# Kernel tuning notes

Hardware: AMD Instinct MI355X
Metric: run time of the kernel (lower is better)

Reference implementation:

```python
import jax, jax.numpy as jnp
import numpy as np

D_MODEL = 1024
NHEAD = 16
WINDOW = 128


def setup_inputs() -> dict:
    key = jax.random.key(0)
    ks = jax.random.split(key, 7)
    B, L, D = 4, 4096, D_MODEL
    s = 0.02
    return {
        "q": jax.random.normal(ks[0], (B, L, D), jnp.float32),
        "k": jax.random.normal(ks[1], (B, L, D), jnp.float32),
        "v": jax.random.normal(ks[2], (B, L, D), jnp.float32),
        "in_proj_w": jax.random.normal(ks[3], (3 * D, D), jnp.float32) * s,
        "in_proj_b": jnp.zeros((3 * D,), jnp.float32),
        "out_w": jax.random.normal(ks[4], (D, D), jnp.float32) * s,
        "out_b": jnp.zeros((D,), jnp.float32),
    }


def reference(q, k, v, in_proj_w, in_proj_b, out_w, out_b):
    B, L, D = q.shape
    H, W = NHEAD, WINDOW
    hd = D // H
    nW = L // W
    Wq, Wk, Wv = in_proj_w[:D], in_proj_w[D:2 * D], in_proj_w[2 * D:]
    bq, bk, bv = in_proj_b[:D], in_proj_b[D:2 * D], in_proj_b[2 * D:]
    # shared per-window projections (same weights every window, as in nn.MultiheadAttention)
    qp = (q @ Wq.T + bq).reshape(B, nW, W, H, hd)
    kp = (k @ Wk.T + bk).reshape(B, nW, W, H, hd)
    vp = (v @ Wv.T + bv).reshape(B, nW, W, H, hd)
    scale = 1.0 / np.sqrt(hd).astype(np.float32)
    # block-diagonal attention: scores only within each window n
    scores = jnp.einsum("bnqhd,bnkhd->bnhqk", qp, kp) * scale  # [B,nW,H,W,W]
    attn = jax.nn.softmax(scores, axis=-1)
    out = jnp.einsum("bnhqk,bnkhd->bnqhd", attn, vp).reshape(B, L, D)
    return out @ out_w.T + out_b
```

## Files before the change

### kernel.cpp

```cpp
#include <hip/hip_runtime.h>

#define M_TOK 16384
#define DM    1024

typedef __bf16 bf16x8 __attribute__((ext_vector_type(8)));
typedef float  f32x4  __attribute__((ext_vector_type(4)));
typedef unsigned short us8 __attribute__((ext_vector_type(8)));
typedef unsigned short us4 __attribute__((ext_vector_type(4)));

__device__ __forceinline__ unsigned short f2bf(float f) {
    unsigned u = __float_as_uint(f);
    u += 0x7FFFu + ((u >> 16) & 1u);
    return (unsigned short)(u >> 16);
}

__device__ __forceinline__ void gl2lds16(const unsigned short* g, unsigned short* l) {
    __builtin_amdgcn_global_load_lds(
        (const __attribute__((address_space(1))) unsigned int*)g,
        (__attribute__((address_space(3))) unsigned int*)l, 16, 0, 0);
}

__global__ __launch_bounds__(256) void conv_f2b(
    const float* __restrict__ src, unsigned short* __restrict__ dst, int n8)
{
    int i = blockIdx.x * blockDim.x + threadIdx.x;
    int stride = gridDim.x * blockDim.x;
    for (; i < n8; i += stride) {
        const float4* s = (const float4*)(src + (size_t)i * 8);
        float4 a = s[0], b = s[1];
        us8 o;
        o[0] = f2bf(a.x); o[1] = f2bf(a.y); o[2] = f2bf(a.z); o[3] = f2bf(a.w);
        o[4] = f2bf(b.x); o[5] = f2bf(b.y); o[6] = f2bf(b.z); o[7] = f2bf(b.w);
        *(us8*)(dst + (size_t)i * 8) = o;
    }
}

#define GEMM_CORE(A_, B_)                                                      \
    __shared__ unsigned short As[4096];                                        \
    __shared__ unsigned short Bs[4096];                                        \
    const int tid = threadIdx.x, lane = tid & 63, wv = tid >> 6;               \
    const int wrow = (wv >> 1) * 64, wcol = (wv & 1) * 64;                     \
    const int lrow = lane & 15, qd = lane >> 4;                                \
    const int mbase = blockIdx.y * 128, nbase = blockIdx.x * 128;              \
    const int s0 = tid, s1 = tid + 256;                                        \
    const int r0 = s0 >> 2, c0 = (s0 & 3) ^ ((r0 >> 1) & 3);                   \
    const int r1 = s1 >> 2, c1 = (s1 & 3) ^ ((r1 >> 1) & 3);                   \
    const int g0 = r0 * DM + c0 * 8;                                           \
    const int g1 = r1 * DM + c1 * 8;                                           \
    int aslot[4], bslot[4];                                                    \
    _Pragma("unroll")                                                          \
    for (int i = 0; i < 4; ++i) {                                              \
        int ra = wrow + i * 16 + lrow;                                         \
        int rb = wcol + i * 16 + lrow;                                         \
        aslot[i] = ra * 32 + (qd ^ ((ra >> 1) & 3)) * 8;                       \
        bslot[i] = rb * 32 + (qd ^ ((rb >> 1) & 3)) * 8;                       \
    }                                                                          \
    const unsigned short* Ab = (A_) + (size_t)mbase * DM;                      \
    const unsigned short* Bb = (B_) + (size_t)nbase * DM;                      \
    f32x4 acc[4][4] = {};                                                      \
    for (int k0 = 0; k0 < DM; k0 += 32) {                                      \
        __syncthreads();                                                       \
        gl2lds16(Ab + k0 + g0, As + s0 * 8);                                   \
        gl2lds16(Ab + k0 + g1, As + s1 * 8);                                   \
        gl2lds16(Bb + k0 + g0, Bs + s0 * 8);                                   \
        gl2lds16(Bb + k0 + g1, Bs + s1 * 8);                                   \
        __syncthreads();                                                       \
        bf16x8 af[4], bfr[4];                                                  \
        _Pragma("unroll")                                                      \
        for (int i = 0; i < 4; ++i) af[i]  = *(const bf16x8*)(As + aslot[i]);  \
        _Pragma("unroll")                                                      \
        for (int i = 0; i < 4; ++i) bfr[i] = *(const bf16x8*)(Bs + bslot[i]);  \
        _Pragma("unroll")                                                      \
        for (int i = 0; i < 4; ++i)                                            \
            _Pragma("unroll")                                                  \
            for (int j = 0; j < 4; ++j)                                        \
                acc[i][j] = __builtin_amdgcn_mfma_f32_16x16x32_bf16(           \
                    af[i], bfr[j], acc[i][j], 0, 0, 0);                        \
    }

__global__ __launch_bounds__(256) void gemm_bt_qkv(
    const unsigned short* __restrict__ A, const unsigned short* __restrict__ W,
    const float* __restrict__ bias, unsigned short* __restrict__ C, int z)
{
    GEMM_CORE(A, W)
    if (z <= 1) {
        #pragma unroll
        for (int j = 0; j < 4; ++j) {
            int gc = nbase + wcol + j * 16 + lrow;
            int h = gc >> 6, dh = gc & 63;
            float bv = bias[gc];
            #pragma unroll
            for (int i = 0; i < 4; ++i) {
                int gr0 = mbase + wrow + i * 16 + qd * 4;
                int b = gr0 >> 12;
                #pragma unroll
                for (int r = 0; r < 4; ++r) {
                    int tok = (gr0 + r) & 4095;
                    C[(((size_t)b * 16 + h) * 4096 + tok) * 64 + dh] =
                        f2bf(acc[i][j][r] + bv);
                }
            }
        }
    } else {
        #pragma unroll
        for (int j = 0; j < 4; ++j) {
            int gc = nbase + wcol + j * 16 + lrow;
            int h = gc >> 6, dh = gc & 63;
            float bv = bias[gc];
            #pragma unroll
            for (int i = 0; i < 4; ++i) {
                int gr0 = mbase + wrow + i * 16 + qd * 4;
                int b = gr0 >> 12, tok = gr0 & 4095;
                us4 pk;
                #pragma unroll
                for (int r = 0; r < 4; ++r) pk[r] = f2bf(acc[i][j][r] + bv);
                *(us4*)(C + (((size_t)b * 16 + h) * 64 + dh) * 4096 + tok) = pk;
            }
        }
    }
}

__global__ __launch_bounds__(256) void gemm_bt_out(
    const unsigned short* __restrict__ A, const unsigned short* __restrict__ W,
    const float* __restrict__ bias, float* __restrict__ out)
{
    GEMM_CORE(A, W)
    #pragma unroll
    for (int j = 0; j < 4; ++j) {
        int gc = nbase + wcol + j * 16 + lrow;
        float bv = bias[gc];
        #pragma unroll
        for (int i = 0; i < 4; ++i) {
            int gr0 = mbase + wrow + i * 16 + qd * 4;
            #pragma unroll
            for (int r = 0; r < 4; ++r)
                out[(size_t)(gr0 + r) * DM + gc] = acc[i][j][r] + bv;
        }
    }
}

__global__ __launch_bounds__(256) void attn_v2(
    const unsigned short* __restrict__ qh, const unsigned short* __restrict__ kh,
    const unsigned short* __restrict__ vt, unsigned short* __restrict__ aout)
{
    const int gid = blockIdx.x;
    const int h  = gid & 15;
    const int wi = (gid >> 4) & 31;
    const int b  = gid >> 9;
    const int bh = b * 16 + h;

    const unsigned short* Qp = qh + ((size_t)bh * 4096 + wi * 128) * 64;
    const unsigned short* Kp = kh + ((size_t)bh * 4096 + wi * 128) * 64;
    const unsigned short* Vp = vt + (size_t)bh * 64 * 4096 + wi * 128;

    const int tid = threadIdx.x, lane = tid & 63, wv = tid >> 6;
    const int lrow = lane & 15, qd = lane >> 4, kof = qd * 8;

    __shared__ unsigned short Ps[128 * 136];

    f32x4 acc[2][8] = {};
    #pragma unroll
    for (int ki = 0; ki < 2; ++ki) {
        bf16x8 a0 = *(const bf16x8*)(Qp + (wv * 32 +  0 + lrow) * 64 + ki * 32 + kof);
        bf16x8 a1 = *(const bf16x8*)(Qp + (wv * 32 + 16 + lrow) * 64 + ki * 32 + kof);
        #pragma unroll
        for (int ni = 0; ni < 8; ++ni) {
            bf16x8 bb = *(const bf16x8*)(Kp + (ni * 16 + lrow) * 64 + ki * 32 + kof);
            acc[0][ni] = __builtin_amdgcn_mfma_f32_16x16x32_bf16(a0, bb, acc[0][ni], 0, 0, 0);
            acc[1][ni] = __builtin_amdgcn_mfma_f32_16x16x32_bf16(a1, bb, acc[1][ni], 0, 0, 0);
        }
    }

    const float scale = 0.125f;
    #pragma unroll
    for (int mi = 0; mi < 2; ++mi) {
        #pragma unroll
        for (int r = 0; r < 4; ++r) {
            float sc[8];
            float mx = -3.4e38f;
            #pragma unroll
            for (int ni = 0; ni < 8; ++ni) { sc[ni] = acc[mi][ni][r] * scale; mx = fmaxf(mx, sc[ni]); }
            mx = fmaxf(mx, __shfl_xor(mx, 1));
            mx = fmaxf(mx, __shfl_xor(mx, 2));
            mx = fmaxf(mx, __shfl_xor(mx, 4));
            mx = fmaxf(mx, __shfl_xor(mx, 8));
            float sum = 0.f;
            #pragma unroll
            for (int ni = 0; ni < 8; ++ni) { sc[ni] = __expf(sc[ni] - mx); sum += sc[ni]; }
            sum += __shfl_xor(sum, 1);
            sum += __shfl_xor(sum, 2);
            sum += __shfl_xor(sum, 4);
            sum += __shfl_xor(sum, 8);
            float inv = 1.0f / sum;
            #pragma unroll
            for (int ni = 0; ni < 8; ++ni) acc[mi][ni][r] = sc[ni] * inv;
        }
    }

    #pragma unroll
    for (int mi = 0; mi < 2; ++mi)
        #pragma unroll
        for (int ni = 0; ni < 8; ++ni)
            #pragma unroll
            for (int r = 0; r < 4; ++r)
                Ps[(wv * 32 + mi * 16 + qd * 4 + r) * 136 + ni * 16 + lrow] =
                    f2bf(acc[mi][ni][r]);

    f32x4 o[2][4] = {};
    #pragma unroll
    for (int kj = 0; kj < 4; ++kj) {
        bf16x8 a0 = *(const bf16x8*)(Ps + (wv * 32 +  0 + lrow) * 136 + kj * 32 + kof);
        bf16x8 a1 = *(const bf16x8*)(Ps + (wv * 32 + 16 + lrow) * 136 + kj * 32 + kof);
        #pragma unroll
        for (int nd = 0; nd < 4; ++nd) {
            bf16x8 bb = *(const bf16x8*)(Vp + (size_t)(nd * 16 + lrow) * 4096 + kj * 32 + kof);
            o[0][nd] = __builtin_amdgcn_mfma_f32_16x16x32_bf16(a0, bb, o[0][nd], 0, 0, 0);
            o[1][nd] = __builtin_amdgcn_mfma_f32_16x16x32_bf16(a1, bb, o[1][nd], 0, 0, 0);
        }
    }

    #pragma unroll
    for (int mi = 0; mi < 2; ++mi)
        #pragma unroll
        for (int nd = 0; nd < 4; ++nd)
            #pragma unroll
            for (int r = 0; r < 4; ++r) {
                int R = wv * 32 + mi * 16 + qd * 4 + r;
                int c = h * 64 + nd * 16 + lrow;
                aout[(size_t)(b * 4096 + wi * 128 + R) * DM + c] = f2bf(o[mi][nd][r]);
            }
}

__global__ __launch_bounds__(256) void gemm_qkv_v1(
    const float* __restrict__ qin, const float* __restrict__ kin,
    const float* __restrict__ vin, const float* __restrict__ ipw,
    const float* __restrict__ ipb, unsigned short* __restrict__ qkv)
{
    __shared__ unsigned short As[128 * 40];
    __shared__ unsigned short Ws[128 * 40];
    const int z = blockIdx.z;
    const float* A  = (z == 0) ? qin : ((z == 1) ? kin : vin);
    const float* Wp = ipw + (size_t)z * DM * DM;
    const float* bp = ipb + z * DM;
    unsigned short* Cp = qkv + (size_t)z * M_TOK * DM;
    const int mbase = blockIdx.y * 128, nbase = blockIdx.x * 128;
    const int tid = threadIdx.x, lane = tid & 63, wv = tid >> 6;
    const int wrow = (wv >> 1) * 64, wcol = (wv & 1) * 64;
    const int lrow = lane & 15, kof = (lane >> 4) * 8;
    const int srow = tid >> 3, sc4 = tid & 7;
    f32x4 acc[4][4] = {};
    for (int ks = 0; ks < 32; ++ks) {
        const int k0 = ks * 32;
        __syncthreads();
        #pragma unroll
        for (int it = 0; it < 4; ++it) {
            int row = it * 32 + srow;
            float4 av = *(const float4*)(A  + (size_t)(mbase + row) * DM + k0 + sc4 * 4);
            float4 wf = *(const float4*)(Wp + (size_t)(nbase + row) * DM + k0 + sc4 * 4);
            us4 ap, wp4;
            ap[0] = f2bf(av.x); ap[1] = f2bf(av.y); ap[2] = f2bf(av.z); ap[3] = f2bf(av.w);
            wp4[0] = f2bf(wf.x); wp4[1] = f2bf(wf.y); wp4[2] = f2bf(wf.z); wp4[3] = f2bf(wf.w);
            *(us4*)(As + row * 40 + sc4 * 4) = ap;
            *(us4*)(Ws + row * 40 + sc4 * 4) = wp4;
        }
        __syncthreads();
        bf16x8 af[4], bfr[4];
        #pragma unroll
        for (int i = 0; i < 4; ++i) af[i]  = *(const bf16x8*)(As + (wrow + i * 16 + lrow) * 40 + kof);
        #pragma unroll
        for (int i = 0; i < 4; ++i) bfr[i] = *(const bf16x8*)(Ws + (wcol + i * 16 + lrow) * 40 + kof);
        #pragma unroll
        for (int i = 0; i < 4; ++i)
            #pragma unroll
            for (int j = 0; j < 4; ++j)
                acc[i][j] = __builtin_amdgcn_mfma_f32_16x16x32_bf16(af[i], bfr[j], acc[i][j], 0, 0, 0);
    }
    #pragma unroll
    for (int j = 0; j < 4; ++j) {
        int gc = nbase + wcol + j * 16 + lrow;
        float bv = bp[gc];
        #pragma unroll
        for (int i = 0; i < 4; ++i) {
            int gr0 = mbase + wrow + i * 16 + (lane >> 4) * 4;
            #pragma unroll
            for (int r = 0; r < 4; ++r)
                Cp[(size_t)(gr0 + r) * DM + gc] = f2bf(acc[i][j][r] + bv);
        }
    }
}

__global__ __launch_bounds__(256) void gemm_out_v1(
    const unsigned short* __restrict__ x, const float* __restrict__ ow,
    const float* __restrict__ ob, float* __restrict__ out)
{
    __shared__ unsigned short As[128 * 40];
    __shared__ unsigned short Ws[128 * 40];
    const int mbase = blockIdx.y * 128, nbase = blockIdx.x * 128;
    const int tid = threadIdx.x, lane = tid & 63, wv = tid >> 6;
    const int wrow = (wv >> 1) * 64, wcol = (wv & 1) * 64;
    const int lrow = lane & 15, kof = (lane >> 4) * 8;
    const int srow = tid >> 3, sc4 = tid & 7;
    f32x4 acc[4][4] = {};
    for (int ks = 0; ks < 32; ++ks) {
        const int k0 = ks * 32;
        __syncthreads();
        #pragma unroll
        for (int it = 0; it < 4; ++it) {
            int row = it * 32 + srow;
            us4 av = *(const us4*)(x + (size_t)(mbase + row) * DM + k0 + sc4 * 4);
            float4 wf = *(const float4*)(ow + (size_t)(nbase + row) * DM + k0 + sc4 * 4);
            us4 wp4;
            wp4[0] = f2bf(wf.x); wp4[1] = f2bf(wf.y); wp4[2] = f2bf(wf.z); wp4[3] = f2bf(wf.w);
            *(us4*)(As + row * 40 + sc4 * 4) = av;
            *(us4*)(Ws + row * 40 + sc4 * 4) = wp4;
        }
        __syncthreads();
        bf16x8 af[4], bfr[4];
        #pragma unroll
        for (int i = 0; i < 4; ++i) af[i]  = *(const bf16x8*)(As + (wrow + i * 16 + lrow) * 40 + kof);
        #pragma unroll
        for (int i = 0; i < 4; ++i) bfr[i] = *(const bf16x8*)(Ws + (wcol + i * 16 + lrow) * 40 + kof);
        #pragma unroll
        for (int i = 0; i < 4; ++i)
            #pragma unroll
            for (int j = 0; j < 4; ++j)
                acc[i][j] = __builtin_amdgcn_mfma_f32_16x16x32_bf16(af[i], bfr[j], acc[i][j], 0, 0, 0);
    }
    #pragma unroll
    for (int j = 0; j < 4; ++j) {
        int gc = nbase + wcol + j * 16 + lrow;
        float bv = ob[gc];
        #pragma unroll
        for (int i = 0; i < 4; ++i) {
            int gr0 = mbase + wrow + i * 16 + (lane >> 4) * 4;
            #pragma unroll
            for (int r = 0; r < 4; ++r)
                out[(size_t)(gr0 + r) * DM + gc] = acc[i][j][r] + bv;
        }
    }
}

__global__ __launch_bounds__(256) void attn_win_v1(
    const unsigned short* __restrict__ qkv, unsigned short* __restrict__ aout)
{
    const unsigned short* qp = qkv;
    const unsigned short* kp = qkv + (size_t)M_TOK * DM;
    const unsigned short* vp = qkv + 2 * (size_t)M_TOK * DM;
    const int gid = blockIdx.x;
    const int h = gid & 15, wi = (gid >> 4) & 31, b = gid >> 9;
    const size_t rowbase = (size_t)b * 4096 + (size_t)wi * 128;
    const int tid = threadIdx.x, lane = tid & 63, wv = tid >> 6;
    const int lrow = lane & 15, kof = (lane >> 4) * 8;
    __shared__ unsigned short sm[27136];
    unsigned short* Qs = sm;
    unsigned short* Ks = sm + 9216;
    unsigned short* Vt = sm + 18432;
    unsigned short* Ps = sm;
    {
        const int seg = tid & 7;
        #pragma unroll
        for (int it = 0; it < 4; ++it) {
            int r = it * 32 + (tid >> 3);
            size_t g = (rowbase + r) * DM + h * 64 + seg * 8;
            *(int4*)(Qs + r * 72 + seg * 8) = *(const int4*)(qp + g);
            *(int4*)(Ks + r * 72 + seg * 8) = *(const int4*)(kp + g);
        }
        #pragma unroll
        for (int it = 0; it < 4; ++it) {
            int j = tid & 127;
            int sg = it * 2 + (tid >> 7);
            us8 vv = *(const us8*)(vp + (rowbase + j) * DM + h * 64 + sg * 8);
            #pragma unroll
            for (int d = 0; d < 8; ++d) Vt[(sg * 8 + d) * 136 + j] = vv[d];
        }
    }
    __syncthreads();
    f32x4 acc[2][8] = {};
    #pragma unroll
    for (int ki = 0; ki < 2; ++ki) {
        bf16x8 a0 = *(const bf16x8*)(Qs + (wv * 32 +  0 + lrow) * 72 + ki * 32 + kof);
        bf16x8 a1 = *(const bf16x8*)(Qs + (wv * 32 + 16 + lrow) * 72 + ki * 32 + kof);
        #pragma unroll
        for (int ni = 0; ni < 8; ++ni) {
            bf16x8 bb = *(const bf16x8*)(Ks + (ni * 16 + lrow) * 72 + ki * 32 + kof);
            acc[0][ni] = __builtin_amdgcn_mfma_f32_16x16x32_bf16(a0, bb, acc[0][ni], 0, 0, 0);
            acc[1][ni] = __builtin_amdgcn_mfma_f32_16x16x32_bf16(a1, bb, acc[1][ni], 0, 0, 0);
        }
    }
    const float scale = 0.125f;
    #pragma unroll
    for (int mi = 0; mi < 2; ++mi) {
        #pragma unroll
        for (int r = 0; r < 4; ++r) {
            float sc[8];
            float mx = -3.4e38f;
            #pragma unroll
            for (int ni = 0; ni < 8; ++ni) { sc[ni] = acc[mi][ni][r] * scale; mx = fmaxf(mx, sc[ni]); }
            mx = fmaxf(mx, __shfl_xor(mx, 1)); mx = fmaxf(mx, __shfl_xor(mx, 2));
            mx = fmaxf(mx, __shfl_xor(mx, 4)); mx = fmaxf(mx, __shfl_xor(mx, 8));
            float sum = 0.f;
            #pragma unroll
            for (int ni = 0; ni < 8; ++ni) { sc[ni] = __expf(sc[ni] - mx); sum += sc[ni]; }
            sum += __shfl_xor(sum, 1); sum += __shfl_xor(sum, 2);
            sum += __shfl_xor(sum, 4); sum += __shfl_xor(sum, 8);
            float inv = 1.0f / sum;
            #pragma unroll
            for (int ni = 0; ni < 8; ++ni) acc[mi][ni][r] = sc[ni] * inv;
        }
    }
    __syncthreads();
    #pragma unroll
    for (int mi = 0; mi < 2; ++mi)
        #pragma unroll
        for (int ni = 0; ni < 8; ++ni)
            #pragma unroll
            for (int r = 0; r < 4; ++r)
                Ps[(wv * 32 + mi * 16 + (lane >> 4) * 4 + r) * 136 + ni * 16 + lrow] =
                    f2bf(acc[mi][ni][r]);
    __syncthreads();
    f32x4 o[2][4] = {};
    #pragma unroll
    for (int kj = 0; kj < 4; ++kj) {
        bf16x8 a0 = *(const bf16x8*)(Ps + (wv * 32 +  0 + lrow) * 136 + kj * 32 + kof);
        bf16x8 a1 = *(const bf16x8*)(Ps + (wv * 32 + 16 + lrow) * 136 + kj * 32 + kof);
        #pragma unroll
        for (int nd = 0; nd < 4; ++nd) {
            bf16x8 bb = *(const bf16x8*)(Vt + (nd * 16 + lrow) * 136 + kj * 32 + kof);
            o[0][nd] = __builtin_amdgcn_mfma_f32_16x16x32_bf16(a0, bb, o[0][nd], 0, 0, 0);
            o[1][nd] = __builtin_amdgcn_mfma_f32_16x16x32_bf16(a1, bb, o[1][nd], 0, 0, 0);
        }
    }
    #pragma unroll
    for (int mi = 0; mi < 2; ++mi)
        #pragma unroll
        for (int nd = 0; nd < 4; ++nd)
            #pragma unroll
            for (int r = 0; r < 4; ++r) {
                int R = wv * 32 + mi * 16 + (lane >> 4) * 4 + r;
                int c = h * 64 + nd * 16 + lrow;
                aout[(rowbase + R) * DM + c] = f2bf(o[mi][nd][r]);
            }
}

extern "C" void kernel_launch(void* const* d_in, const int* in_sizes, int n_in,
                              void* d_out, int out_size, void* d_ws, size_t ws_size,
                              hipStream_t stream) {
    const float* q   = (const float*)d_in[0];
    const float* k   = (const float*)d_in[1];
    const float* v   = (const float*)d_in[2];
    const float* ipw = (const float*)d_in[3];
    const float* ipb = (const float*)d_in[4];
    const float* ow  = (const float*)d_in[5];
    const float* ob  = (const float*)d_in[6];
    float* out = (float*)d_out;

    const size_t MD = (size_t)M_TOK * DM;
    const size_t WW = (size_t)DM * DM;
    const size_t need = (4 * MD + 3 * WW) * 2;

    if (ws_size >= need) {
        unsigned short* X   = (unsigned short*)d_ws;
        unsigned short* qh  = X + MD;
        unsigned short* kh  = X + 2 * MD;
        unsigned short* vtb = X + 3 * MD;
        unsigned short* Wb  = X + 4 * MD;
        unsigned short* aout = X;
        unsigned short* OwB  = Wb;

        conv_f2b<<<1536, 256, 0, stream>>>(ipw, Wb, (int)(3 * WW / 8));
        conv_f2b<<<8192, 256, 0, stream>>>(q, X, (int)(MD / 8));
        gemm_bt_qkv<<<dim3(8, 128), 256, 0, stream>>>(X, Wb, ipb, qh, 0);
        conv_f2b<<<8192, 256, 0, stream>>>(k, X, (int)(MD / 8));
        gemm_bt_qkv<<<dim3(8, 128), 256, 0, stream>>>(X, Wb + WW, ipb + DM, kh, 1);
        conv_f2b<<<8192, 256, 0, stream>>>(v, X, (int)(MD / 8));
        gemm_bt_qkv<<<dim3(8, 128), 256, 0, stream>>>(X, Wb + 2 * WW, ipb + 2 * DM, vtb, 2);
        conv_f2b<<<512, 256, 0, stream>>>(ow, OwB, (int)(WW / 8));
        attn_v2<<<2048, 256, 0, stream>>>(qh, kh, vtb, aout);
        gemm_bt_out<<<dim3(8, 128), 256, 0, stream>>>(aout, OwB, ob, out);
    } else {
        unsigned short* qkv = (unsigned short*)d_ws;
        const size_t qkv_elems = 3 * MD;
        const size_t need_full = (qkv_elems + MD) * 2;
        unsigned short* aout = (ws_size >= need_full) ? qkv + qkv_elems : qkv;
        gemm_qkv_v1<<<dim3(8, 128, 3), 256, 0, stream>>>(q, k, v, ipw, ipb, qkv);
        attn_win_v1<<<2048, 256, 0, stream>>>(qkv, aout);
        gemm_out_v1<<<dim3(8, 128), 256, 0, stream>>>(aout, ow, ob, out);
    }
}
```

Measured before the change: 495.4 us.

## Replace GEMM core with 256x256 double-buffered LDS pipeline and tile swizzle

The 128x128 single-buffered GEMM with BK=32 becomes a 256x256 tile, 512-thread kernel with BK=64 (two k-substeps). It double-buffers LDS, using explicit vmcnt waits and barriers so global-to-LDS loads overlap the MFMA work. It also swizzles the block-to-tile mapping for L2 locality and raises MFMA issue priority. The aim is to hide load latency and cut barrier overhead per FLOP in the four projection GEMMs. The costs are 128KB of LDS per block and high register pressure (8x4 accumulators), which may limit occupancy, plus fewer blocks (256) for the machine's CUs.

After: 531.9 us. 1.07x slower.

```diff
diff --git a/kernel.cpp b/kernel.cpp
--- a/kernel.cpp
+++ b/kernel.cpp
@@ -35,106 +35,146 @@
     }
 }
 
-#define GEMM_CORE(A_, B_)                                                      \
-    __shared__ unsigned short As[4096];                                        \
-    __shared__ unsigned short Bs[4096];                                        \
-    const int tid = threadIdx.x, lane = tid & 63, wv = tid >> 6;               \
-    const int wrow = (wv >> 1) * 64, wcol = (wv & 1) * 64;                     \
-    const int lrow = lane & 15, qd = lane >> 4;                                \
-    const int mbase = blockIdx.y * 128, nbase = blockIdx.x * 128;              \
-    const int s0 = tid, s1 = tid + 256;                                        \
-    const int r0 = s0 >> 2, c0 = (s0 & 3) ^ ((r0 >> 1) & 3);                   \
-    const int r1 = s1 >> 2, c1 = (s1 & 3) ^ ((r1 >> 1) & 3);                   \
-    const int g0 = r0 * DM + c0 * 8;                                           \
-    const int g1 = r1 * DM + c1 * 8;                                           \
-    int aslot[4], bslot[4];                                                    \
-    _Pragma("unroll")                                                          \
-    for (int i = 0; i < 4; ++i) {                                              \
-        int ra = wrow + i * 16 + lrow;                                         \
-        int rb = wcol + i * 16 + lrow;                                         \
-        aslot[i] = ra * 32 + (qd ^ ((ra >> 1) & 3)) * 8;                       \
-        bslot[i] = rb * 32 + (qd ^ ((rb >> 1) & 3)) * 8;                       \
-    }                                                                          \
-    const unsigned short* Ab = (A_) + (size_t)mbase * DM;                      \
-    const unsigned short* Bb = (B_) + (size_t)nbase * DM;                      \
-    f32x4 acc[4][4] = {};                                                      \
-    for (int k0 = 0; k0 < DM; k0 += 32) {                                      \
-        __syncthreads();                                                       \
-        gl2lds16(Ab + k0 + g0, As + s0 * 8);                                   \
-        gl2lds16(Ab + k0 + g1, As + s1 * 8);                                   \
-        gl2lds16(Bb + k0 + g0, Bs + s0 * 8);                                   \
-        gl2lds16(Bb + k0 + g1, Bs + s1 * 8);                                   \
-        __syncthreads();                                                       \
-        bf16x8 af[4], bfr[4];                                                  \
-        _Pragma("unroll")                                                      \
-        for (int i = 0; i < 4; ++i) af[i]  = *(const bf16x8*)(As + aslot[i]);  \
-        _Pragma("unroll")                                                      \
-        for (int i = 0; i < 4; ++i) bfr[i] = *(const bf16x8*)(Bs + bslot[i]);  \
-        _Pragma("unroll")                                                      \
-        for (int i = 0; i < 4; ++i)                                            \
-            _Pragma("unroll")                                                  \
-            for (int j = 0; j < 4; ++j)                                        \
-                acc[i][j] = __builtin_amdgcn_mfma_f32_16x16x32_bf16(           \
-                    af[i], bfr[j], acc[i][j], 0, 0, 0);                        \
-    }
-
-__global__ __launch_bounds__(256) void gemm_bt_qkv(
+#define PIPE_WAIT8() asm volatile("s_waitcnt vmcnt(8)" ::: "memory")
+#define PIPE_WAIT0() asm volatile("s_waitcnt vmcnt(0)" ::: "memory")
+
+#define STAGE(G_, k0_, Lb_)                                                  \
+    _Pragma("unroll")                                                        \
+    for (int j = 0; j < 4; ++j) {                                            \
+        int p = tid + j * 512;                                               \
+        int kkp = p >> 10, rem = p & 1023;                                   \
+        int r = rem >> 2, cp = rem & 3;                                      \
+        int cl = cp ^ ((r >> 1) & 3);                                        \
+        gl2lds16((G_) + (size_t)r * DM + (k0_) + kkp * 32 + cl * 8,          \
+                 (Lb_) + p * 8);                                             \
+    }
+
+#define COMPUTE(bi_)                                                         \
+    _Pragma("unroll")                                                        \
+    for (int kk = 0; kk < 2; ++kk) {                                         \
+        bf16x8 af[8], bb[4];                                                 \
+        _Pragma("unroll")                                                    \
+        for (int mi = 0; mi < 8; ++mi)                                       \
+            af[mi] = *(const bf16x8*)(smem[bi_] + kk * 8192 + sA + mi * 512);\
+        _Pragma("unroll")                                                    \
+        for (int ni = 0; ni < 4; ++ni)                                       \
+            bb[ni] = *(const bf16x8*)(smem[bi_] + kk * 8192 + sB + ni * 512);\
+        __builtin_amdgcn_s_setprio(1);                                       \
+        _Pragma("unroll")                                                    \
+        for (int mi = 0; mi < 8; ++mi)                                       \
+            _Pragma("unroll")                                                \
+            for (int ni = 0; ni < 4; ++ni)                                   \
+                acc[mi][ni] = __builtin_amdgcn_mfma_f32_16x16x32_bf16(       \
+                    af[mi], bb[ni], acc[mi][ni], 0, 0, 0);                   \
+        __builtin_amdgcn_s_setprio(0);                                       \
+    }
+
+#define GEMM256_CORE(A_, B_)                                                 \
+    __shared__ unsigned short smem[2][32768];                    \
+    const int tid = threadIdx.x, lane = tid & 63, wv = tid >> 6;             \
+    const int wm = wv >> 2, wn = wv & 3;                                     \
+    const int lrow = lane & 15, qd = lane >> 4;                              \
+    const int orig = blockIdx.y * 4 + blockIdx.x;     \
+    const int swz  = (orig & 7) * 32 + (orig >> 3);                          \
+    const int mbase = (swz >> 2) * 256, nbase = (swz & 3) * 256;             \
+    const unsigned short* Ab = (A_) + (size_t)mbase * DM;                    \
+    const unsigned short* Bb = (B_) + (size_t)nbase * DM;                    \
+              \
+    const int sA = (qd ^ ((lrow >> 1) & 3)) * 8 + (wm * 128 + lrow) * 32;    \
+    const int sB = (qd ^ ((lrow >> 1) & 3)) * 8 + (wn * 64 + lrow) * 32      \
+                   + 16384;                                                  \
+    f32x4 acc[8][4] = {};                                                    \
+                                                \
+    STAGE(Ab, 0, smem[0]);  STAGE(Bb, 0, smem[0] + 16384);                   \
+    STAGE(Ab, 64, smem[1]); STAGE(Bb, 64, smem[1] + 16384);                  \
+    PIPE_WAIT8();                                                            \
+    __builtin_amdgcn_s_barrier();                                            \
+    __builtin_amdgcn_sched_barrier(0);                                       \
+    _Pragma("unroll 1")                                                      \
+    for (int t = 0; t < 16; t += 2) {                                        \
+        COMPUTE(0);                                                          \
+        __builtin_amdgcn_sched_barrier(0);                                   \
+        __builtin_amdgcn_s_barrier();       \
+        if (t + 2 < 16) {                                                    \
+            STAGE(Ab, (t + 2) * 64, smem[0]);                                \
+            STAGE(Bb, (t + 2) * 64, smem[0] + 16384);                        \
+            PIPE_WAIT8();                               \
+        } else {                                                             \
+            PIPE_WAIT0();                                    \
+        }                                                                    \
+        __builtin_amdgcn_s_barrier();                                        \
+        __builtin_amdgcn_sched_barrier(0);                                   \
+        COMPUTE(1);                                                          \
+        __builtin_amdgcn_sched_barrier(0);                                   \
+        __builtin_amdgcn_s_barrier();                                        \
+        if (t + 3 < 16) {                                                    \
+            STAGE(Ab, (t + 3) * 64, smem[1]);                                \
+            STAGE(Bb, (t + 3) * 64, smem[1] + 16384);                        \
+            PIPE_WAIT8();                               \
+        } else if (t + 2 < 16) {                                             \
+            PIPE_WAIT0();                                                    \
+        }                                                                    \
+        __builtin_amdgcn_s_barrier();                                        \
+        __builtin_amdgcn_sched_barrier(0);                                   \
+    }
+
+__global__ __launch_bounds__(512, 2) void gemm256_qkv(
     const unsigned short* __restrict__ A, const unsigned short* __restrict__ W,
     const float* __restrict__ bias, unsigned short* __restrict__ C, int z)
 {
-    GEMM_CORE(A, W)
+    GEMM256_CORE(A, W)
     if (z <= 1) {
         #pragma unroll
-        for (int j = 0; j < 4; ++j) {
-            int gc = nbase + wcol + j * 16 + lrow;
+        for (int ni = 0; ni < 4; ++ni) {
+            int gc = nbase + wn * 64 + ni * 16 + lrow;
             int h = gc >> 6, dh = gc & 63;
             float bv = bias[gc];
             #pragma unroll
-            for (int i = 0; i < 4; ++i) {
-                int gr0 = mbase + wrow + i * 16 + qd * 4;
+            for (int mi = 0; mi < 8; ++mi) {
+                int gr0 = mbase + wm * 128 + mi * 16 + qd * 4;
                 int b = gr0 >> 12;
                 #pragma unroll
                 for (int r = 0; r < 4; ++r) {
                     int tok = (gr0 + r) & 4095;
                     C[(((size_t)b * 16 + h) * 4096 + tok) * 64 + dh] =
-                        f2bf(acc[i][j][r] + bv);
+                        f2bf(acc[mi][ni][r] + bv);
                 }
             }
         }
     } else {
         #pragma unroll
-        for (int j = 0; j < 4; ++j) {
-            int gc = nbase + wcol + j * 16 + lrow;
+        for (int ni = 0; ni < 4; ++ni) {
+            int gc = nbase + wn * 64 + ni * 16 + lrow;
             int h = gc >> 6, dh = gc & 63;
             float bv = bias[gc];
             #pragma unroll
-            for (int i = 0; i < 4; ++i) {
-                int gr0 = mbase + wrow + i * 16 + qd * 4;
+            for (int mi = 0; mi < 8; ++mi) {
+                int gr0 = mbase + wm * 128 + mi * 16 + qd * 4;
                 int b = gr0 >> 12, tok = gr0 & 4095;
                 us4 pk;
                 #pragma unroll
-                for (int r = 0; r < 4; ++r) pk[r] = f2bf(acc[i][j][r] + bv);
+                for (int r = 0; r < 4; ++r) pk[r] = f2bf(acc[mi][ni][r] + bv);
                 *(us4*)(C + (((size_t)b * 16 + h) * 64 + dh) * 4096 + tok) = pk;
             }
         }
     }
 }
 
-__global__ __launch_bounds__(256) void gemm_bt_out(
+__global__ __launch_bounds__(512, 2) void gemm256_out(
     const unsigned short* __restrict__ A, const unsigned short* __restrict__ W,
     const float* __restrict__ bias, float* __restrict__ out)
 {
-    GEMM_CORE(A, W)
-    #pragma unroll
-    for (int j = 0; j < 4; ++j) {
-        int gc = nbase + wcol + j * 16 + lrow;
+    GEMM256_CORE(A, W)
+    #pragma unroll
+    for (int ni = 0; ni < 4; ++ni) {
+        int gc = nbase + wn * 64 + ni * 16 + lrow;
         float bv = bias[gc];
         #pragma unroll
-        for (int i = 0; i < 4; ++i) {
-            int gr0 = mbase + wrow + i * 16 + qd * 4;
+        for (int mi = 0; mi < 8; ++mi) {
+            int gr0 = mbase + wm * 128 + mi * 16 + qd * 4;
             #pragma unroll
             for (int r = 0; r < 4; ++r)
-                out[(size_t)(gr0 + r) * DM + gc] = acc[i][j][r] + bv;
+                out[(size_t)(gr0 + r) * DM + gc] = acc[mi][ni][r] + bv;
         }
     }
 }
@@ -469,14 +509,14 @@
 
         conv_f2b<<<1536, 256, 0, stream>>>(ipw, Wb, (int)(3 * WW / 8));
         conv_f2b<<<8192, 256, 0, stream>>>(q, X, (int)(MD / 8));
-        gemm_bt_qkv<<<dim3(8, 128), 256, 0, stream>>>(X, Wb, ipb, qh, 0);
+        gemm256_qkv<<<dim3(4, 64), 512, 0, stream>>>(X, Wb, ipb, qh, 0);
         conv_f2b<<<8192, 256, 0, stream>>>(k, X, (int)(MD / 8));
-        gemm_bt_qkv<<<dim3(8, 128), 256, 0, stream>>>(X, Wb + WW, ipb + DM, kh, 1);
+        gemm256_qkv<<<dim3(4, 64), 512, 0, stream>>>(X, Wb + WW, ipb + DM, kh, 1);
         conv_f2b<<<8192, 256, 0, stream>>>(v, X, (int)(MD / 8));
-        gemm_bt_qkv<<<dim3(8, 128), 256, 0, stream>>>(X, Wb + 2 * WW, ipb + 2 * DM, vtb, 2);
+        gemm256_qkv<<<dim3(4, 64), 512, 0, stream>>>(X, Wb + 2 * WW, ipb + 2 * DM, vtb, 2);
         conv_f2b<<<512, 256, 0, stream>>>(ow, OwB, (int)(WW / 8));
         attn_v2<<<2048, 256, 0, stream>>>(qh, kh, vtb, aout);
-        gemm_bt_out<<<dim3(8, 128), 256, 0, stream>>>(aout, OwB, ob, out);
+        gemm256_out<<<dim3(4, 64), 512, 0, stream>>>(aout, OwB, ob, out);
     } else {
         unsigned short* qkv = (unsigned short*)d_ws;
         const size_t qkv_elems = 3 * MD;
```
